# Kernel optimization log

Hardware: AMD Instinct MI355X
Metric: run time of the kernel (lower is better)

## Reference

```python
import jax, jax.numpy as jnp
import numpy as np

N = 200_000
E = 3_200_000
H = 24

def setup_inputs() -> dict:
    key = jax.random.key(0)
    ks = jax.random.split(key, 12)
    s = 1.0 / np.sqrt(H).astype(np.float32)
    u = lambda k, shape: jax.random.uniform(k, shape, jnp.float32, -s, s)
    return {
        "x": jax.random.normal(ks[0], (N,), jnp.float32),
        "h0": jax.random.normal(ks[1], (1, N, H), jnp.float32) * 0.1,
        "c0": jax.random.normal(ks[2], (1, N, H), jnp.float32) * 0.1,
        "edge_index": jax.random.randint(ks[3], (2, E), 0, N, dtype=jnp.int32),
        "w_ih": u(ks[4], (4 * H, 1)),
        "w_hh": u(ks[5], (4 * H, H)),
        "b_ih": u(ks[6], (4 * H,)),
        "b_hh": u(ks[7], (4 * H,)),
        "gcn_w": u(ks[8], (H, H)),
        "gcn_b": u(ks[9], (H,)),
        "lin_w": u(ks[10], (1, H)),
        "lin_b": u(ks[11], (1,)),
    }

def reference(x, h0, c0, edge_index, w_ih, w_hh, b_ih, b_hh, gcn_w, gcn_b, lin_w, lin_b):
    # --- LSTM single step (seq_len=1, batch=N, input_size=1, hidden=H) ---
    h_prev = h0[0]  # [N, H]
    c_prev = c0[0]  # [N, H]
    # gates in torch order: input, forget, cell(g), output
    gates = x[:, None] * w_ih[:, 0][None, :] + b_ih + h_prev @ w_hh.T + b_hh  # [N, 4H]
    i, f, g, o = jnp.split(gates, 4, axis=-1)
    i = jax.nn.sigmoid(i); f = jax.nn.sigmoid(f); o = jax.nn.sigmoid(o); g = jnp.tanh(g)
    c = f * c_prev + i * g
    h = o * jnp.tanh(c)  # [N, H] -- LSTM output == new hidden state

    # --- GCNConv(24,24): symmetric norm with self loops (PyG default) ---
    xw = h @ gcn_w.T  # [N, H]
    src, dst = edge_index[0], edge_index[1]
    deg = jax.ops.segment_sum(jnp.ones(src.shape, xw.dtype), dst, num_segments=N) + 1.0
    dinv = jax.lax.rsqrt(deg)                      # deg >= 1 due to self loops
    norm = dinv[src] * dinv[dst]                   # [E]
    msg = xw[src] * norm[:, None]                  # [E, H]
    agg = jax.ops.segment_sum(msg, dst, num_segments=N)
    agg = agg + xw * (dinv * dinv)[:, None]        # self-loop edges
    conv = agg + gcn_b                             # [N, H]

    # --- Linear(24,1) + elementwise gate ---
    out = (conv @ lin_w.T + lin_b).reshape(-1)     # [N]
    return x * out, h[None], c[None]
```

## Files before the change

kernel.cpp:

```cpp
#include <hip/hip_runtime.h>
#include <math.h>

#define H 24
#define B0 4096
#define B0_SHIFT 12
#define MAXNB 64
#define NBPAD 65
#define P 8
#define CAP 70000
#define CSTRIDE 16
#define K1_EPB 4096

__device__ __forceinline__ float sigmoidf_(float v) {
    return 1.0f / (1.0f + __expf(-v));
}
__device__ __forceinline__ float tanhf_(float v) {
    return 1.0f - 2.0f / (__expf(2.0f * v) + 1.0f);
}

__global__ void init_kernel(unsigned* __restrict__ cursors,
                            const float* __restrict__ gcn_w,
                            const float* __restrict__ gcn_b,
                            const float* __restrict__ lin_w,
                            const float* __restrict__ lin_b,
                            float* __restrict__ g, float* __restrict__ cb, int NB) {
    int t = threadIdx.x;
    if (t < H) {
        float acc = 0.0f;
        for (int j = 0; j < H; j++) acc = fmaf(lin_w[j], gcn_w[j * H + t], acc);
        g[t] = acc;
    }
    if (t == 32) {
        float c = lin_b[0];
        for (int j = 0; j < H; j++) c = fmaf(gcn_b[j], lin_w[j], c);
        *cb = c;
    }
    if (t < MAXNB) cursors[t * CSTRIDE] = (unsigned)t * CAP;
}

__global__ __launch_bounds__(256) void scatter_kernel(
    const int* __restrict__ src, const int* __restrict__ dst,
    unsigned* __restrict__ cursors, unsigned* __restrict__ pedge, int E, int NB)
{
    __shared__ unsigned cnt[4][NBPAD];
    __shared__ unsigned c3[4][NBPAD];
    __shared__ unsigned base[4][NBPAD];

    const int tid = threadIdx.x;
    const int w = tid >> 6;
    const int start = blockIdx.x * K1_EPB;
    const bool full = (E - start) >= K1_EPB;
    const int ebase = start + tid * 16;

    for (int i = tid; i < 4 * NBPAD; i += 256) {
        (&cnt[0][0])[i] = 0;
        (&c3[0][0])[i] = 0;
    }
    __syncthreads();

    unsigned dreg[16];
    if (full) {
        const uint4* dp = (const uint4*)(dst + ebase);
        #pragma unroll
        for (int q = 0; q < 4; q++) {
            uint4 v = dp[q];
            dreg[4*q+0] = v.x; dreg[4*q+1] = v.y; dreg[4*q+2] = v.z; dreg[4*q+3] = v.w;
        }
        #pragma unroll
        for (int q = 0; q < 16; q++)
            atomicAdd(&cnt[w][dreg[q] >> B0_SHIFT], 1u);
    } else {
        #pragma unroll
        for (int q = 0; q < 16; q++) {
            int e = ebase + q;
            if (e < E) {
                unsigned d = (unsigned)dst[e];
                dreg[q] = d;
                atomicAdd(&cnt[w][d >> B0_SHIFT], 1u);
            } else dreg[q] = 0xFFFFFFFFu;
        }
    }
    __syncthreads();

    if (tid < NB) {
        unsigned c0 = cnt[0][tid], c1 = cnt[1][tid], c2 = cnt[2][tid], cw3 = cnt[3][tid];
        unsigned tot = c0 + c1 + c2 + cw3;
        unsigned gb = tot ? atomicAdd(&cursors[tid * CSTRIDE], tot) : 0u;
        base[0][tid] = gb;
        base[1][tid] = gb + c0;
        base[2][tid] = gb + c0 + c1;
        base[3][tid] = gb + c0 + c1 + c2;
    }
    __syncthreads();

    if (full) {
        unsigned sreg[16];
        const uint4* sp = (const uint4*)(src + ebase);
        #pragma unroll
        for (int q = 0; q < 4; q++) {
            uint4 v = sp[q];
            sreg[4*q+0] = v.x; sreg[4*q+1] = v.y; sreg[4*q+2] = v.z; sreg[4*q+3] = v.w;
        }
        #pragma unroll
        for (int q = 0; q < 16; q++) {
            unsigned d = dreg[q];
            unsigned b = d >> B0_SHIFT;
            unsigned slot = atomicAdd(&c3[w][b], 1u);
            unsigned idx  = base[w][b] + slot;
            if (idx < (b + 1u) * CAP)
                pedge[idx] = (sreg[q] << B0_SHIFT) | (d & (B0 - 1));
        }
    } else {
        #pragma unroll
        for (int q = 0; q < 16; q++) {
            int e = ebase + q;
            if (e < E) {
                unsigned d = dreg[q];
                unsigned b = d >> B0_SHIFT;
                unsigned slot = atomicAdd(&c3[w][b], 1u);
                unsigned idx  = base[w][b] + slot;
                if (idx < (b + 1u) * CAP)
                    pedge[idx] = ((unsigned)src[e] << B0_SHIFT) | (d & (B0 - 1));
            }
        }
    }
}

__global__ __launch_bounds__(256) void deghist_kernel(
    const unsigned* __restrict__ pedge, const unsigned* __restrict__ cursors,
    unsigned short* __restrict__ degp, int NB, int NPAD)
{
    __shared__ unsigned h[B0];
    int b = blockIdx.x % NB, p = blockIdx.x / NB;
    for (int i = threadIdx.x; i < B0; i += 256) h[i] = 0;
    __syncthreads();
    unsigned base = (unsigned)b * CAP;
    unsigned sz = cursors[b * CSTRIDE] - base; if (sz > CAP) sz = CAP;
    unsigned chunk = (sz + P - 1) / P;
    unsigned s0 = p * chunk;
    unsigned s1 = s0 + chunk; if (s1 > sz) s1 = sz;
    for (unsigned i = s0 + threadIdx.x; i < s1; i += 256)
        atomicAdd(&h[pedge[base + i] & (B0 - 1)], 1u);
    __syncthreads();
    unsigned short* out = degp + (size_t)p * NPAD + (size_t)b * B0;
    for (int i = threadIdx.x; i < B0; i += 256) out[i] = (unsigned short)h[i];
}

__global__ __launch_bounds__(256) void node_kernel(
    const float* __restrict__ x, const float* __restrict__ h0, const float* __restrict__ c0,
    const float* __restrict__ w_ih, const float* __restrict__ w_hh,
    const float* __restrict__ b_ih, const float* __restrict__ b_hh,
    const float* __restrict__ g,
    float* __restrict__ out_h, float* __restrict__ out_c,
    float* __restrict__ y, int N)
{
    __shared__ float ws[96 * 24];
    __shared__ float swih[96];
    __shared__ float sbs[96];
    __shared__ float sg[24];

    #pragma unroll 3
    for (int i = threadIdx.x; i < 96 * 24; i += 256) ws[i] = w_hh[i];
    if (threadIdx.x < 96) {
        swih[threadIdx.x] = w_ih[threadIdx.x];
        sbs[threadIdx.x]  = b_ih[threadIdx.x] + b_hh[threadIdx.x];
    } else if (threadIdx.x >= 128 && threadIdx.x < 152) {
        sg[threadIdx.x - 128] = g[threadIdx.x - 128];
    }
    __syncthreads();

    int tid = blockIdx.x * 256 + threadIdx.x;
    int pr  = tid >> 2;
    int n0  = pr * 2;
    if (n0 >= N) return;
    int n1  = n0 + 1;
    int t   = tid & 3;
    int k0  = 6 * t;

    float hp0[H], hp1[H];
    {
        const float4* a4 = (const float4*)(h0 + (size_t)n0 * H);
        const float4* b4 = (const float4*)(h0 + (size_t)n1 * H);
        #pragma unroll
        for (int q = 0; q < 6; q++) {
            float4 va = a4[q], vb = b4[q];
            hp0[4*q+0] = va.x; hp0[4*q+1] = va.y; hp0[4*q+2] = va.z; hp0[4*q+3] = va.w;
            hp1[4*q+0] = vb.x; hp1[4*q+1] = vb.y; hp1[4*q+2] = vb.z; hp1[4*q+3] = vb.w;
        }
    }
    float cp0[6], cp1[6];
    {
        const float2* a2 = (const float2*)(c0 + (size_t)n0 * H + k0);
        const float2* b2 = (const float2*)(c0 + (size_t)n1 * H + k0);
        #pragma unroll
        for (int q = 0; q < 3; q++) {
            float2 va = a2[q], vb = b2[q];
            cp0[2*q] = va.x; cp0[2*q+1] = va.y;
            cp1[2*q] = vb.x; cp1[2*q+1] = vb.y;
        }
    }
    float xv0 = x[n0], xv1 = x[n1];
    float yv0 = 0.0f, yv1 = 0.0f;

    #pragma unroll
    for (int i = 0; i < 6; i++) {
        int k = k0 + i;
        float bi = sbs[k], bf = sbs[k + 24], bg = sbs[k + 48], bo = sbs[k + 72];
        float wik = swih[k], wfk = swih[k + 24], wgk = swih[k + 48], wok = swih[k + 72];
        float gi0 = fmaf(xv0, wik, bi), gi1 = fmaf(xv1, wik, bi);
        float gf0 = fmaf(xv0, wfk, bf), gf1 = fmaf(xv1, wfk, bf);
        float gg0 = fmaf(xv0, wgk, bg), gg1 = fmaf(xv1, wgk, bg);
        float go0 = fmaf(xv0, wok, bo), go1 = fmaf(xv1, wok, bo);
        const float* w0 = ws + k * 24;
        #pragma unroll
        for (int c = 0; c < 6; c++) {
            float4 wi = *(const float4*)(w0 + 4*c);
            float4 wf = *(const float4*)(w0 + 576  + 4*c);
            float4 wg = *(const float4*)(w0 + 1152 + 4*c);
            float4 wo = *(const float4*)(w0 + 1728 + 4*c);
            float a0 = hp0[4*c+0], a1 = hp0[4*c+1], a2 = hp0[4*c+2], a3 = hp0[4*c+3];
            float d0 = hp1[4*c+0], d1 = hp1[4*c+1], d2 = hp1[4*c+2], d3 = hp1[4*c+3];
            gi0 = fmaf(a0, wi.x, gi0); gi0 = fmaf(a1, wi.y, gi0);
            gi0 = fmaf(a2, wi.z, gi0); gi0 = fmaf(a3, wi.w, gi0);
            gi1 = fmaf(d0, wi.x, gi1); gi1 = fmaf(d1, wi.y, gi1);
            gi1 = fmaf(d2, wi.z, gi1); gi1 = fmaf(d3, wi.w, gi1);
            gf0 = fmaf(a0, wf.x, gf0); gf0 = fmaf(a1, wf.y, gf0);
            gf0 = fmaf(a2, wf.z, gf0); gf0 = fmaf(a3, wf.w, gf0);
            gf1 = fmaf(d0, wf.x, gf1); gf1 = fmaf(d1, wf.y, gf1);
            gf1 = fmaf(d2, wf.z, gf1); gf1 = fmaf(d3, wf.w, gf1);
            gg0 = fmaf(a0, wg.x, gg0); gg0 = fmaf(a1, wg.y, gg0);
            gg0 = fmaf(a2, wg.z, gg0); gg0 = fmaf(a3, wg.w, gg0);
            gg1 = fmaf(d0, wg.x, gg1); gg1 = fmaf(d1, wg.y, gg1);
            gg1 = fmaf(d2, wg.z, gg1); gg1 = fmaf(d3, wg.w, gg1);
            go0 = fmaf(a0, wo.x, go0); go0 = fmaf(a1, wo.y, go0);
            go0 = fmaf(a2, wo.z, go0); go0 = fmaf(a3, wo.w, go0);
            go1 = fmaf(d0, wo.x, go1); go1 = fmaf(d1, wo.y, go1);
            go1 = fmaf(d2, wo.z, go1); go1 = fmaf(d3, wo.w, go1);
        }
        gi0 = sigmoidf_(gi0); gf0 = sigmoidf_(gf0); go0 = sigmoidf_(go0); gg0 = tanhf_(gg0);
        gi1 = sigmoidf_(gi1); gf1 = sigmoidf_(gf1); go1 = sigmoidf_(go1); gg1 = tanhf_(gg1);
        float c_0 = fmaf(gf0, cp0[i], gi0 * gg0);
        float c_1 = fmaf(gf1, cp1[i], gi1 * gg1);
        float h_0 = go0 * tanhf_(c_0);
        float h_1 = go1 * tanhf_(c_1);
        out_c[(size_t)n0 * H + k] = c_0;
        out_c[(size_t)n1 * H + k] = c_1;
        out_h[(size_t)n0 * H + k] = h_0;
        out_h[(size_t)n1 * H + k] = h_1;
        float gk = sg[k];
        yv0 = fmaf(h_0, gk, yv0);
        yv1 = fmaf(h_1, gk, yv1);
    }
    yv0 += __shfl_xor(yv0, 1); yv0 += __shfl_xor(yv0, 2);
    yv1 += __shfl_xor(yv1, 1); yv1 += __shfl_xor(yv1, 2);
    if (t == 0) y[n0] = yv0;
    if (t == 1) y[n1] = yv1;
}

__global__ __launch_bounds__(256) void z_kernel(
    const float* __restrict__ y, const unsigned short* __restrict__ degp, int NPAD,
    float* __restrict__ dinv, float* __restrict__ z, int N)
{
    int n = blockIdx.x * 256 + threadIdx.x;
    if (n >= N) return;
    unsigned dg = 0;
    #pragma unroll
    for (int p = 0; p < P; p++) dg += degp[(size_t)p * NPAD + n];
    float di = rsqrtf((float)dg + 1.0f);
    dinv[n] = di;
    z[n] = di * y[n];
}

__global__ __launch_bounds__(256) void acchist_kernel(
    const unsigned* __restrict__ pedge, const unsigned* __restrict__ cursors,
    const float* __restrict__ z, float* __restrict__ accp, int NB, int NPAD)
{
    __shared__ float h[B0];
    int b = blockIdx.x % NB, p = blockIdx.x / NB;
    for (int i = threadIdx.x; i < B0; i += 256) h[i] = 0.0f;
    __syncthreads();
    unsigned base = (unsigned)b * CAP;
    unsigned sz = cursors[b * CSTRIDE] - base; if (sz > CAP) sz = CAP;
    unsigned chunk = (sz + P - 1) / P;
    unsigned s0 = p * chunk;
    unsigned s1 = s0 + chunk; if (s1 > sz) s1 = sz;
    for (unsigned i = s0 + threadIdx.x; i < s1; i += 256) {
        unsigned v = pedge[base + i];
        atomicAdd(&h[v & (B0 - 1)], z[v >> B0_SHIFT]);
    }
    __syncthreads();
    float* out = accp + (size_t)p * NPAD + (size_t)b * B0;
    for (int i = threadIdx.x; i < B0; i += 256) out[i] = h[i];
}

__global__ __launch_bounds__(256) void final_kernel(
    const float* __restrict__ x, const float* __restrict__ accp, int NPAD,
    const float* __restrict__ y, const float* __restrict__ dinv,
    const float* __restrict__ cb, float* __restrict__ out, int N)
{
    int n = blockIdx.x * blockDim.x + threadIdx.x;
    if (n >= N) return;
    float a = 0.0f;
    #pragma unroll
    for (int p = 0; p < P; p++) a += accp[(size_t)p * NPAD + n];
    float di = dinv[n];
    float s  = di * a + di * di * y[n] + cb[0];
    out[n] = x[n] * s;
}

extern "C" void kernel_launch(void* const* d_in, const int* in_sizes, int n_in,
                              void* d_out, int out_size, void* d_ws, size_t ws_size,
                              hipStream_t stream) {
    const float* x     = (const float*)d_in[0];
    const float* h0    = (const float*)d_in[1];
    const float* c0    = (const float*)d_in[2];
    const int*   ei    = (const int*)d_in[3];
    const float* w_ih  = (const float*)d_in[4];
    const float* w_hh  = (const float*)d_in[5];
    const float* b_ih  = (const float*)d_in[6];
    const float* b_hh  = (const float*)d_in[7];
    const float* gcn_w = (const float*)d_in[8];
    const float* gcn_b = (const float*)d_in[9];
    const float* lin_w = (const float*)d_in[10];
    const float* lin_b = (const float*)d_in[11];

    const int N = in_sizes[0];
    const int E = in_sizes[3] / 2;
    const int* src = ei;
    const int* dst = ei + E;

    const int NB   = (N + B0 - 1) / B0;
    const int NPAD = NB * B0;

    float* out_gate = (float*)d_out;
    float* out_h    = out_gate + N;
    float* out_c    = out_h + (size_t)N * H;

    char* w = (char*)d_ws;
    unsigned*       pedge   = (unsigned*)w;       w += (size_t)NB * CAP * 4;
    unsigned short* degp    = (unsigned short*)w; w += (size_t)P * NPAD * 2;
    float*          accp    = (float*)w;          w += (size_t)P * NPAD * 4;
    float*          y       = (float*)w;          w += (size_t)N * 4;
    float*          zv      = (float*)w;          w += (size_t)N * 4;
    float*          dinv    = (float*)w;          w += (size_t)N * 4;
    float*          g       = (float*)w;          w += H * 4;
    float*          cb      = (float*)w;          w += 4;
    unsigned*       cursors = (unsigned*)w;       w += MAXNB * CSTRIDE * 4;

    init_kernel   <<<1, 64, 0, stream>>>(cursors, gcn_w, gcn_b, lin_w, lin_b, g, cb, NB);
    scatter_kernel<<<(E + K1_EPB - 1) / K1_EPB, 256, 0, stream>>>(src, dst, cursors,
                                                                  pedge, E, NB);
    deghist_kernel<<<NB * P, 256, 0, stream>>>(pedge, cursors, degp, NB, NPAD);
    node_kernel   <<<((size_t)N * 2 + 255) / 256, 256, 0, stream>>>(
                       x, h0, c0, w_ih, w_hh, b_ih, b_hh, g, out_h, out_c, y, N);
    z_kernel      <<<(N + 255) / 256, 256, 0, stream>>>(y, degp, NPAD, dinv, zv, N);
    acchist_kernel<<<NB * P, 256, 0, stream>>>(pedge, cursors, zv, accp, NB, NPAD);
    final_kernel  <<<(N + 255) / 256, 256, 0, stream>>>(x, accp, NPAD, y, dinv, cb,
                                                        out_gate, N);
}
```

Baseline: 113.6 us.

## Map one node per thread in LSTM kernel and read weights from global

```diff
diff --git a/kernel.cpp b/kernel.cpp
--- a/kernel.cpp
+++ b/kernel.cpp
@@ -154,107 +154,47 @@
     float* __restrict__ out_h, float* __restrict__ out_c,
     float* __restrict__ y, int N)
 {
-    __shared__ float ws[96 * 24];
-    __shared__ float swih[96];
-    __shared__ float sbs[96];
-    __shared__ float sg[24];
-
-    #pragma unroll 3
-    for (int i = threadIdx.x; i < 96 * 24; i += 256) ws[i] = w_hh[i];
-    if (threadIdx.x < 96) {
-        swih[threadIdx.x] = w_ih[threadIdx.x];
-        sbs[threadIdx.x]  = b_ih[threadIdx.x] + b_hh[threadIdx.x];
-    } else if (threadIdx.x >= 128 && threadIdx.x < 152) {
-        sg[threadIdx.x - 128] = g[threadIdx.x - 128];
-    }
-    __syncthreads();
-
-    int tid = blockIdx.x * 256 + threadIdx.x;
-    int pr  = tid >> 2;
-    int n0  = pr * 2;
-    if (n0 >= N) return;
-    int n1  = n0 + 1;
-    int t   = tid & 3;
-    int k0  = 6 * t;
-
-    float hp0[H], hp1[H];
+    int n = blockIdx.x * 256 + threadIdx.x;
+    if (n >= N) return;
+
+    float hp[H];
     {
-        const float4* a4 = (const float4*)(h0 + (size_t)n0 * H);
-        const float4* b4 = (const float4*)(h0 + (size_t)n1 * H);
+        const float4* h4 = (const float4*)(h0 + (size_t)n * H);
         #pragma unroll
         for (int q = 0; q < 6; q++) {
-            float4 va = a4[q], vb = b4[q];
-            hp0[4*q+0] = va.x; hp0[4*q+1] = va.y; hp0[4*q+2] = va.z; hp0[4*q+3] = va.w;
-            hp1[4*q+0] = vb.x; hp1[4*q+1] = vb.y; hp1[4*q+2] = vb.z; hp1[4*q+3] = vb.w;
-        }
-    }
-    float cp0[6], cp1[6];
-    {
-        const float2* a2 = (const float2*)(c0 + (size_t)n0 * H + k0);
-        const float2* b2 = (const float2*)(c0 + (size_t)n1 * H + k0);
-        #pragma unroll
-        for (int q = 0; q < 3; q++) {
-            float2 va = a2[q], vb = b2[q];
-            cp0[2*q] = va.x; cp0[2*q+1] = va.y;
-            cp1[2*q] = vb.x; cp1[2*q+1] = vb.y;
-        }
-    }
-    float xv0 = x[n0], xv1 = x[n1];
-    float yv0 = 0.0f, yv1 = 0.0f;
-
-    #pragma unroll
-    for (int i = 0; i < 6; i++) {
-        int k = k0 + i;
-        float bi = sbs[k], bf = sbs[k + 24], bg = sbs[k + 48], bo = sbs[k + 72];
-        float wik = swih[k], wfk = swih[k + 24], wgk = swih[k + 48], wok = swih[k + 72];
-        float gi0 = fmaf(xv0, wik, bi), gi1 = fmaf(xv1, wik, bi);
-        float gf0 = fmaf(xv0, wfk, bf), gf1 = fmaf(xv1, wfk, bf);
-        float gg0 = fmaf(xv0, wgk, bg), gg1 = fmaf(xv1, wgk, bg);
-        float go0 = fmaf(xv0, wok, bo), go1 = fmaf(xv1, wok, bo);
-        const float* w0 = ws + k * 24;
-        #pragma unroll
-        for (int c = 0; c < 6; c++) {
-            float4 wi = *(const float4*)(w0 + 4*c);
-            float4 wf = *(const float4*)(w0 + 576  + 4*c);
-            float4 wg = *(const float4*)(w0 + 1152 + 4*c);
-            float4 wo = *(const float4*)(w0 + 1728 + 4*c);
-            float a0 = hp0[4*c+0], a1 = hp0[4*c+1], a2 = hp0[4*c+2], a3 = hp0[4*c+3];
-            float d0 = hp1[4*c+0], d1 = hp1[4*c+1], d2 = hp1[4*c+2], d3 = hp1[4*c+3];
-            gi0 = fmaf(a0, wi.x, gi0); gi0 = fmaf(a1, wi.y, gi0);
-            gi0 = fmaf(a2, wi.z, gi0); gi0 = fmaf(a3, wi.w, gi0);
-            gi1 = fmaf(d0, wi.x, gi1); gi1 = fmaf(d1, wi.y, gi1);
-            gi1 = fmaf(d2, wi.z, gi1); gi1 = fmaf(d3, wi.w, gi1);
-            gf0 = fmaf(a0, wf.x, gf0); gf0 = fmaf(a1, wf.y, gf0);
-            gf0 = fmaf(a2, wf.z, gf0); gf0 = fmaf(a3, wf.w, gf0);
-            gf1 = fmaf(d0, wf.x, gf1); gf1 = fmaf(d1, wf.y, gf1);
-            gf1 = fmaf(d2, wf.z, gf1); gf1 = fmaf(d3, wf.w, gf1);
-            gg0 = fmaf(a0, wg.x, gg0); gg0 = fmaf(a1, wg.y, gg0);
-            gg0 = fmaf(a2, wg.z, gg0); gg0 = fmaf(a3, wg.w, gg0);
-            gg1 = fmaf(d0, wg.x, gg1); gg1 = fmaf(d1, wg.y, gg1);
-            gg1 = fmaf(d2, wg.z, gg1); gg1 = fmaf(d3, wg.w, gg1);
-            go0 = fmaf(a0, wo.x, go0); go0 = fmaf(a1, wo.y, go0);
-            go0 = fmaf(a2, wo.z, go0); go0 = fmaf(a3, wo.w, go0);
-            go1 = fmaf(d0, wo.x, go1); go1 = fmaf(d1, wo.y, go1);
-            go1 = fmaf(d2, wo.z, go1); go1 = fmaf(d3, wo.w, go1);
-        }
-        gi0 = sigmoidf_(gi0); gf0 = sigmoidf_(gf0); go0 = sigmoidf_(go0); gg0 = tanhf_(gg0);
-        gi1 = sigmoidf_(gi1); gf1 = sigmoidf_(gf1); go1 = sigmoidf_(go1); gg1 = tanhf_(gg1);
-        float c_0 = fmaf(gf0, cp0[i], gi0 * gg0);
-        float c_1 = fmaf(gf1, cp1[i], gi1 * gg1);
-        float h_0 = go0 * tanhf_(c_0);
-        float h_1 = go1 * tanhf_(c_1);
-        out_c[(size_t)n0 * H + k] = c_0;
-        out_c[(size_t)n1 * H + k] = c_1;
-        out_h[(size_t)n0 * H + k] = h_0;
-        out_h[(size_t)n1 * H + k] = h_1;
-        float gk = sg[k];
-        yv0 = fmaf(h_0, gk, yv0);
-        yv1 = fmaf(h_1, gk, yv1);
-    }
-    yv0 += __shfl_xor(yv0, 1); yv0 += __shfl_xor(yv0, 2);
-    yv1 += __shfl_xor(yv1, 1); yv1 += __shfl_xor(yv1, 2);
-    if (t == 0) y[n0] = yv0;
-    if (t == 1) y[n1] = yv1;
+            float4 v = h4[q];
+            hp[4*q+0] = v.x; hp[4*q+1] = v.y; hp[4*q+2] = v.z; hp[4*q+3] = v.w;
+        }
+    }
+    float xv = x[n];
+    float yv = 0.0f;
+    const float* cin  = c0 + (size_t)n * H;
+    float*       hout = out_h + (size_t)n * H;
+    float*       cout = out_c + (size_t)n * H;
+
+    #pragma unroll 4
+    for (int k = 0; k < H; k++) {
+        float gi = fmaf(xv, w_ih[k],      b_ih[k]      + b_hh[k]);
+        float gf = fmaf(xv, w_ih[k + 24], b_ih[k + 24] + b_hh[k + 24]);
+        float gg = fmaf(xv, w_ih[k + 48], b_ih[k + 48] + b_hh[k + 48]);
+        float go = fmaf(xv, w_ih[k + 72], b_ih[k + 72] + b_hh[k + 72]);
+        const float* wr0 = w_hh + (size_t)k * H;
+        #pragma unroll
+        for (int j = 0; j < H; j++) {
+            float hj = hp[j];
+            gi = fmaf(hj, wr0[j],        gi);
+            gf = fmaf(hj, wr0[j + 576],  gf);
+            gg = fmaf(hj, wr0[j + 1152], gg);
+            go = fmaf(hj, wr0[j + 1728], go);
+        }
+        gi = sigmoidf_(gi); gf = sigmoidf_(gf); go = sigmoidf_(go); gg = tanhf_(gg);
+        float c_ = fmaf(gf, cin[k], gi * gg);
+        float h_ = go * tanhf_(c_);
+        cout[k] = c_;
+        hout[k] = h_;
+        yv = fmaf(h_, g[k], yv);
+    }
+    y[n] = yv;
 }
 
 __global__ __launch_bounds__(256) void z_kernel(
@@ -351,8 +291,8 @@
     scatter_kernel<<<(E + K1_EPB - 1) / K1_EPB, 256, 0, stream>>>(src, dst, cursors,
                                                                   pedge, E, NB);
     deghist_kernel<<<NB * P, 256, 0, stream>>>(pedge, cursors, degp, NB, NPAD);
-    node_kernel   <<<((size_t)N * 2 + 255) / 256, 256, 0, stream>>>(
-                       x, h0, c0, w_ih, w_hh, b_ih, b_hh, g, out_h, out_c, y, N);
+    node_kernel   <<<(N + 255) / 256, 256, 0, stream>>>(x, h0, c0, w_ih, w_hh, b_ih, b_hh,
+                                                        g, out_h, out_c, y, N);
     z_kernel      <<<(N + 255) / 256, 256, 0, stream>>>(y, degp, NPAD, dinv, zv, N);
     acchist_kernel<<<NB * P, 256, 0, stream>>>(pedge, cursors, zv, accp, NB, NPAD);
     final_kernel  <<<(N + 255) / 256, 256, 0, stream>>>(x, accp, NPAD, y, dinv, cb,
```

After: 146.6 us. +29.0%, slower.
